# Optimization experiments

Hardware: AMD Instinct MI355X
Metric: run time of the kernel (lower is better)

Reference implementation:

```python
import jax, jax.numpy as jnp
import numpy as np

H = 64   # LSTM hidden size
NL = 8   # LSTM layers
B, T = 2048, 64


def setup_inputs() -> dict:
    key = jax.random.key(0)
    ks = jax.random.split(key, 18)
    r = lambda i, shape, s=0.1: jax.random.normal(ks[i], shape, dtype=jnp.float32) * s
    return {
        "x": r(0, (B, T, 2), 1.0),
        "w1": r(1, (16, 2)), "b1": r(2, (16,)),
        "w2": r(3, (16, 16)), "b2": r(4, (16,)),
        "w_ih0": r(5, (4 * H, 16)), "w_hh0": r(6, (4 * H, H)),
        "b_ih0": r(7, (4 * H,)), "b_hh0": r(8, (4 * H,)),
        "w_ih": r(9, (NL - 1, 4 * H, H)), "w_hh": r(10, (NL - 1, 4 * H, H)),
        "b_ih": r(11, (NL - 1, 4 * H)), "b_hh": r(12, (NL - 1, 4 * H)),
        "wo1": r(13, (32, H)), "bo1": r(14, (32,)),
        "wo2": r(15, (4, 32)), "bo2": r(16, (4,)),
    }


def _lstm_layer(x, w_ih, w_hh, b):
    # x: [B, T, I]; torch gate order: i, f, g, o
    bsz = x.shape[0]
    xg = jnp.einsum('bti,gi->btg', x, w_ih) + b  # [B, T, 4H] precomputed input gates

    def step(carry, xg_t):
        h, c = carry
        gates = xg_t + h @ w_hh.T
        i, f, g, o = jnp.split(gates, 4, axis=-1)
        i = jax.nn.sigmoid(i); f = jax.nn.sigmoid(f)
        g = jnp.tanh(g); o = jax.nn.sigmoid(o)
        c = f * c + i * g
        h = o * jnp.tanh(c)
        return (h, c), h

    h0 = jnp.zeros((bsz, H), x.dtype)
    _, hs = jax.lax.scan(step, (h0, h0), jnp.swapaxes(xg, 0, 1))  # [T, B, H]
    return jnp.swapaxes(hs, 0, 1)


def reference(x, w1, b1, w2, b2, w_ih0, w_hh0, b_ih0, b_hh0,
              w_ih, w_hh, b_ih, b_hh, wo1, bo1, wo2, bo2):
    # action-input MLP: 2 -> 16 -> relu -> 16
    h = jax.nn.relu(x @ w1.T + b1) @ w2.T + b2
    # 8-layer LSTM, hidden 64
    h = _lstm_layer(h, w_ih0, w_hh0, b_ih0 + b_hh0)
    for l in range(NL - 1):
        h = _lstm_layer(h, w_ih[l], w_hh[l], b_ih[l] + b_hh[l])
    # output MLP: 64 -> 32 -> relu -> 4
    return jax.nn.relu(h @ wo1.T + bo1) @ wo2.T + bo2
```

## Files before the change

### kernel.cpp

```cpp
#include <hip/hip_runtime.h>


#define BATCH 2048
#define TT 64
#define HH 64
#define LDP 136

typedef short bf16x8 __attribute__((ext_vector_type(8)));
typedef float f32x4 __attribute__((ext_vector_type(4)));

__device__ __forceinline__ float sigmoid_fast(float x) {
    return __builtin_amdgcn_rcpf(1.f + __expf(-x));
}
__device__ __forceinline__ float tanh_fast(float x) {
    float e = __expf(-2.f * x);
    e = fminf(e, 1e30f);
    return (1.f - e) * __builtin_amdgcn_rcpf(1.f + e);
}
__device__ __forceinline__ void split2(float x, unsigned short& hi, unsigned short& lo) {
    const unsigned u = __float_as_uint(x);
    hi = (unsigned short)(u >> 16);
    const float r = x - __uint_as_float(u & 0xFFFF0000u);
    lo = (unsigned short)(__float_as_uint(r) >> 16);
}

__global__ __launch_bounds__(256)
void mlp_in_kernel(const float* __restrict__ x,
                   const float* __restrict__ w1, const float* __restrict__ b1,
                   const float* __restrict__ w2, const float* __restrict__ b2,
                   float* __restrict__ out) {
    const int gid = blockIdx.x * 256 + threadIdx.x;
    const float x0 = x[gid * 2 + 0];
    const float x1 = x[gid * 2 + 1];
    float hid[16];
#pragma unroll
    for (int j = 0; j < 16; ++j) {
        float v = fmaf(x1, w1[j * 2 + 1], fmaf(x0, w1[j * 2 + 0], b1[j]));
        hid[j] = fmaxf(0.f, v);
    }
    float o[16];
#pragma unroll
    for (int oo = 0; oo < 16; ++oo) {
        float acc = b2[oo];
#pragma unroll
        for (int j = 0; j < 16; ++j) acc = fmaf(hid[j], w2[oo * 16 + j], acc);
        o[oo] = acc;
    }
    float4* op = (float4*)(out + gid * 16);
#pragma unroll
    for (int q = 0; q < 4; ++q) {
        float4 v;
        v.x = o[q * 4 + 0]; v.y = o[q * 4 + 1]; v.z = o[q * 4 + 2]; v.w = o[q * 4 + 3];
        op[q] = v;
    }
}

template <int I, int IPAD>
__global__ __launch_bounds__(512, 2)
void lstm_layer(const float* __restrict__ xin,
                const float* __restrict__ w_ih, const float* __restrict__ w_hh,
                const float* __restrict__ b_ih, const float* __restrict__ b_hh,
                float* __restrict__ hout) {
    constexpr int K = IPAD + 64;
    constexpr int KT = K / 32;
    __shared__ unsigned short ph[2][16 * LDP];
    __shared__ unsigned short pl[2][16 * LDP];
    __shared__ float gsw[8][32][8];

    const int tid = threadIdx.x;
    const int wv = tid >> 6, lane = tid & 63, l16 = lane & 15, quad = lane >> 4;
    const int base = blockIdx.x * 8;

    for (int e = tid; e < 16 * LDP; e += 512) {
        ph[0][e] = 0; pl[0][e] = 0; ph[1][e] = 0; pl[1][e] = 0;
    }

    bf16x8 bhi[KT][2], blo[KT][2];
    float bsum[2];
#pragma unroll
    for (int ntl = 0; ntl < 2; ++ntl) {
        const int gate = ntl * 2 + (l16 >> 3);
        const int n = gate * 64 + 8 * wv + (l16 & 7);
        bsum[ntl] = b_ih[n] + b_hh[n];
#pragma unroll
        for (int kt = 0; kt < KT; ++kt) {
#pragma unroll
            for (int j = 0; j < 8; ++j) {
                const int k = kt * 32 + quad * 8 + j;
                float w = 0.f;
                if (k < I) w = w_ih[n * I + k];
                else if (k >= IPAD) w = w_hh[n * 64 + (k - IPAD)];
                unsigned short h_, l_;
                split2(w, h_, l_);
                bhi[kt][ntl][j] = (short)h_;
                blo[kt][ntl][j] = (short)l_;
            }
        }
    }

    float c = 0.f;
    const int cm = lane >> 3, cjj = lane & 7;
    const int cj = 8 * wv + cjj;

    const int am = (I == 64) ? (tid >> 6) : (tid >> 4);
    const int ak = (I == 64) ? (tid & 63) : (tid & 15);
    const bool stg = (I == 64) ? true : (tid < 128);

    float xr = 0.f;
    if (stg) xr = xin[((size_t)(base + am) * TT + 0) * I + ak];
    if (stg) {
        unsigned short h_, l_;
        split2(xr, h_, l_);
        ph[0][am * LDP + ak] = h_;
        pl[0][am * LDP + ak] = l_;
    }
    if (stg) xr = xin[((size_t)(base + am) * TT + 1) * I + ak];
    __syncthreads();

    for (int t = 0; t < TT; ++t) {
        const int pb = t & 1;
        const unsigned short* php = ph[pb];
        const unsigned short* plp = pl[pb];
        unsigned short* phn = ph[pb ^ 1];
        unsigned short* pln = pl[pb ^ 1];

        f32x4 a0[2], a1[2], a2[2];
#pragma unroll
        for (int ntl = 0; ntl < 2; ++ntl) {
            a0[ntl][0] = bsum[ntl]; a0[ntl][1] = bsum[ntl];
            a0[ntl][2] = bsum[ntl]; a0[ntl][3] = bsum[ntl];
            a1[ntl] = (f32x4){0.f, 0.f, 0.f, 0.f};
            a2[ntl] = (f32x4){0.f, 0.f, 0.f, 0.f};
        }
#pragma unroll
        for (int kt = 0; kt < KT; ++kt) {
            const int aoff = l16 * LDP + kt * 32 + quad * 8;
            const bf16x8 ahi = *(const bf16x8*)&php[aoff];
            const bf16x8 alo = *(const bf16x8*)&plp[aoff];
#pragma unroll
            for (int ntl = 0; ntl < 2; ++ntl) {
                a0[ntl] = __builtin_amdgcn_mfma_f32_16x16x32_bf16(ahi, bhi[kt][ntl], a0[ntl], 0, 0, 0);
                a1[ntl] = __builtin_amdgcn_mfma_f32_16x16x32_bf16(alo, bhi[kt][ntl], a1[ntl], 0, 0, 0);
                a2[ntl] = __builtin_amdgcn_mfma_f32_16x16x32_bf16(ahi, blo[kt][ntl], a2[ntl], 0, 0, 0);
            }
        }
        if (quad < 2) {
#pragma unroll
            for (int ntl = 0; ntl < 2; ++ntl) {
                const f32x4 s = (a0[ntl] + a1[ntl]) + a2[ntl];
                *(f32x4*)&gsw[wv][ntl * 16 + l16][quad * 4] = s;
            }
        }

        const float gi = gsw[wv][0 * 8 + cjj][cm];
        const float gf = gsw[wv][1 * 8 + cjj][cm];
        const float gg = gsw[wv][2 * 8 + cjj][cm];
        const float go = gsw[wv][3 * 8 + cjj][cm];
        const float iv = sigmoid_fast(gi), fv = sigmoid_fast(gf);
        const float gv = tanh_fast(gg), ov = sigmoid_fast(go);
        c = fv * c + iv * gv;
        const float h = ov * tanh_fast(c);
        {
            unsigned short h_, l_;
            split2(h, h_, l_);
            phn[cm * LDP + IPAD + cj] = h_;
            pln[cm * LDP + IPAD + cj] = l_;
            hout[((size_t)(base + cm) * TT + t) * HH + cj] = h;
        }

        if (stg) {
            unsigned short h_, l_;
            split2(xr, h_, l_);
            phn[am * LDP + ak] = h_;
            pln[am * LDP + ak] = l_;
            const int tp = (t + 2) & (TT - 1);
            xr = xin[((size_t)(base + am) * TT + tp) * I + ak];
        }
        __syncthreads();
    }
}

__global__ __launch_bounds__(256)
void mlp_out_kernel(const float* __restrict__ hin,
                    const float* __restrict__ wo1, const float* __restrict__ bo1,
                    const float* __restrict__ wo2, const float* __restrict__ bo2,
                    float* __restrict__ out) {
    __shared__ __align__(16) float wo1_s[32 * 64];
    __shared__ float bo1_s[32];
    __shared__ float wo2_s[4 * 32];
    __shared__ float bo2_s[4];
    const int tid = threadIdx.x;
    for (int e = tid; e < 32 * 64; e += 256) wo1_s[e] = wo1[e];
    if (tid < 32) bo1_s[tid] = bo1[tid];
    if (tid < 128) wo2_s[tid] = wo2[tid];
    if (tid < 4) bo2_s[tid] = bo2[tid];
    __syncthreads();

    const int gid = blockIdx.x * 256 + tid;
    const float4* hv = (const float4*)(hin + gid * 64);
    float4 h[16];
#pragma unroll
    for (int q = 0; q < 16; ++q) h[q] = hv[q];

    float m1[32];
#pragma unroll
    for (int o = 0; o < 32; ++o) {
        float acc = bo1_s[o];
        const float4* wrow = (const float4*)(wo1_s + o * 64);
#pragma unroll
        for (int q = 0; q < 16; ++q) {
            const float4 w = wrow[q];
            acc = fmaf(h[q].x, w.x, acc);
            acc = fmaf(h[q].y, w.y, acc);
            acc = fmaf(h[q].z, w.z, acc);
            acc = fmaf(h[q].w, w.w, acc);
        }
        m1[o] = fmaxf(0.f, acc);
    }
    float r[4];
#pragma unroll
    for (int q = 0; q < 4; ++q) {
        float acc = bo2_s[q];
#pragma unroll
        for (int o = 0; o < 32; ++o) acc = fmaf(m1[o], wo2_s[q * 32 + o], acc);
        r[q] = acc;
    }
    float4 res;
    res.x = r[0]; res.y = r[1]; res.z = r[2]; res.w = r[3];
    ((float4*)out)[gid] = res;
}

extern "C" void kernel_launch(void* const* d_in, const int* in_sizes, int n_in,
                              void* d_out, int out_size, void* d_ws, size_t ws_size,
                              hipStream_t stream) {
    const float* x     = (const float*)d_in[0];
    const float* w1    = (const float*)d_in[1];
    const float* b1    = (const float*)d_in[2];
    const float* w2    = (const float*)d_in[3];
    const float* b2    = (const float*)d_in[4];
    const float* w_ih0 = (const float*)d_in[5];
    const float* w_hh0 = (const float*)d_in[6];
    const float* b_ih0 = (const float*)d_in[7];
    const float* b_hh0 = (const float*)d_in[8];
    const float* w_ih  = (const float*)d_in[9];
    const float* w_hh  = (const float*)d_in[10];
    const float* b_ih  = (const float*)d_in[11];
    const float* b_hh  = (const float*)d_in[12];
    const float* wo1   = (const float*)d_in[13];
    const float* bo1   = (const float*)d_in[14];
    const float* wo2   = (const float*)d_in[15];
    const float* bo2   = (const float*)d_in[16];

    float* buf_mlp = (float*)d_ws;
    float* bufA = buf_mlp + (size_t)BATCH * TT * 16;
    float* bufB = bufA + (size_t)BATCH * TT * 64;

    const int nbt_blocks = (BATCH * TT) / 256;

    mlp_in_kernel<<<nbt_blocks, 256, 0, stream>>>(x, w1, b1, w2, b2, buf_mlp);

    lstm_layer<16, 32><<<BATCH / 8, 512, 0, stream>>>(buf_mlp, w_ih0, w_hh0, b_ih0, b_hh0, bufA);

    const float* cur = bufA;
    float* nxt = bufB;
    for (int l = 0; l < 7; ++l) {
        lstm_layer<64, 64><<<BATCH / 8, 512, 0, stream>>>(
            cur, w_ih + (size_t)l * 256 * 64, w_hh + (size_t)l * 256 * 64,
            b_ih + (size_t)l * 256, b_hh + (size_t)l * 256, nxt);
        const float* tmp = nxt;
        nxt = (float*)cur;
        cur = tmp;
    }

    mlp_out_kernel<<<nbt_blocks, 256, 0, stream>>>(cur, wo1, bo1, wo2, bo2, (float*)d_out);
}
```

Measured before the change: 572.1 us.

## Fuse eight LSTM layers into one wavefront-pipelined persistent kernel

```diff
diff --git a/kernel.cpp b/kernel.cpp
--- a/kernel.cpp
+++ b/kernel.cpp
@@ -5,9 +5,12 @@
 #define TT 64
 #define HH 64
 #define LDP 136
+#define GRP 32
+#define RING 8
 
 typedef short bf16x8 __attribute__((ext_vector_type(8)));
 typedef float f32x4 __attribute__((ext_vector_type(4)));
+typedef unsigned short u16x4 __attribute__((ext_vector_type(4)));
 
 __device__ __forceinline__ float sigmoid_fast(float x) {
     return __builtin_amdgcn_rcpf(1.f + __expf(-x));
@@ -55,128 +58,186 @@
     }
 }
 
-template <int I, int IPAD>
 __global__ __launch_bounds__(512, 2)
-void lstm_layer(const float* __restrict__ xin,
-                const float* __restrict__ w_ih, const float* __restrict__ w_hh,
-                const float* __restrict__ b_ih, const float* __restrict__ b_hh,
-                float* __restrict__ hout) {
-    constexpr int K = IPAD + 64;
-    constexpr int KT = K / 32;
-    __shared__ unsigned short ph[2][16 * LDP];
-    __shared__ unsigned short pl[2][16 * LDP];
-    __shared__ float gsw[8][32][8];
-
+void lstm_wavefront(const float* __restrict__ xmlp,
+                    const float* __restrict__ w_ih0, const float* __restrict__ w_hh0,
+                    const float* __restrict__ b_ih0, const float* __restrict__ b_hh0,
+                    const float* __restrict__ w_ih, const float* __restrict__ w_hh,
+                    const float* __restrict__ b_ih, const float* __restrict__ b_hh,
+                    unsigned* __restrict__ hring,
+                    float* __restrict__ houtf,
+                    int* __restrict__ prog,
+                    int* __restrict__ cons)
+{
+    const int bid = blockIdx.x;
+    const int l = bid >> 5, g = bid & (GRP - 1);
     const int tid = threadIdx.x;
     const int wv = tid >> 6, lane = tid & 63, l16 = lane & 15, quad = lane >> 4;
-    const int base = blockIdx.x * 8;
-
-    for (int e = tid; e < 16 * LDP; e += 512) {
+    const int mw = wv >> 2, nw = wv & 3;
+
+    const int I    = (l == 0) ? 16 : 64;
+    const int IPAD = (l == 0) ? 32 : 64;
+    const int KT   = (l == 0) ? 3 : 4;
+    const float* wih = (l == 0) ? w_ih0 : (w_ih + (size_t)(l - 1) * 256 * 64);
+    const float* whh = (l == 0) ? w_hh0 : (w_hh + (size_t)(l - 1) * 256 * 64);
+    const float* bi  = (l == 0) ? b_ih0 : (b_ih + (l - 1) * 256);
+    const float* bh  = (l == 0) ? b_hh0 : (b_hh + (l - 1) * 256);
+
+    __shared__ unsigned short ph[2][64 * LDP];
+    __shared__ unsigned short pl[2][64 * LDP];
+
+    for (int e = tid; e < 64 * LDP; e += 512) {
         ph[0][e] = 0; pl[0][e] = 0; ph[1][e] = 0; pl[1][e] = 0;
     }
 
-    bf16x8 bhi[KT][2], blo[KT][2];
-    float bsum[2];
-#pragma unroll
-    for (int ntl = 0; ntl < 2; ++ntl) {
-        const int gate = ntl * 2 + (l16 >> 3);
-        const int n = gate * 64 + 8 * wv + (l16 & 7);
-        bsum[ntl] = b_ih[n] + b_hh[n];
-#pragma unroll
-        for (int kt = 0; kt < KT; ++kt) {
-#pragma unroll
-            for (int j = 0; j < 8; ++j) {
-                const int k = kt * 32 + quad * 8 + j;
-                float w = 0.f;
-                if (k < I) w = w_ih[n * I + k];
-                else if (k >= IPAD) w = w_hh[n * 64 + (k - IPAD)];
-                unsigned short h_, l_;
-                split2(w, h_, l_);
-                bhi[kt][ntl][j] = (short)h_;
-                blo[kt][ntl][j] = (short)l_;
-            }
-        }
-    }
-
-    float c = 0.f;
-    const int cm = lane >> 3, cjj = lane & 7;
-    const int cj = 8 * wv + cjj;
-
-    const int am = (I == 64) ? (tid >> 6) : (tid >> 4);
-    const int ak = (I == 64) ? (tid & 63) : (tid & 15);
-    const bool stg = (I == 64) ? true : (tid < 128);
-
-    float xr = 0.f;
-    if (stg) xr = xin[((size_t)(base + am) * TT + 0) * I + ak];
-    if (stg) {
-        unsigned short h_, l_;
-        split2(xr, h_, l_);
-        ph[0][am * LDP + ak] = h_;
-        pl[0][am * LDP + ak] = l_;
-    }
-    if (stg) xr = xin[((size_t)(base + am) * TT + 1) * I + ak];
+    bf16x8 bhi[4][4], blo[4][4];
+    float bsum[4];
+#pragma unroll
+    for (int gt = 0; gt < 4; ++gt) {
+        const int n = gt * 64 + 16 * nw + l16;
+        bsum[gt] = bi[n] + bh[n];
+#pragma unroll
+        for (int kt = 0; kt < 4; ++kt) {
+            bf16x8 vh = {0, 0, 0, 0, 0, 0, 0, 0};
+            bf16x8 vl = {0, 0, 0, 0, 0, 0, 0, 0};
+            if (kt < KT) {
+#pragma unroll
+                for (int j = 0; j < 8; ++j) {
+                    const int k = kt * 32 + quad * 8 + j;
+                    float w = 0.f;
+                    if (k < I) w = wih[n * I + k];
+                    else if (k >= IPAD) w = whh[n * 64 + (k - IPAD)];
+                    unsigned short h_, l_;
+                    split2(w, h_, l_);
+                    vh[j] = (short)h_;
+                    vl[j] = (short)l_;
+                }
+            }
+            bhi[kt][gt] = vh;
+            blo[kt][gt] = vl;
+        }
+    }
+
+    float cst[2][4];
+#pragma unroll
+    for (int q = 0; q < 4; ++q) { cst[0][q] = 0.f; cst[1][q] = 0.f; }
+
+    int* myprog = prog + l * GRP + g;
+    int* upprog = prog + (l > 0 ? (l - 1) : 0) * GRP + g;
+    int* mycons = cons + l * GRP + g;
+    int* dncons = cons + (l < 7 ? (l + 1) : 7) * GRP + g;
+    const unsigned* hr_src = hring + ((size_t)((l > 0 ? l - 1 : 0) * GRP + g)) * (RING * 4096);
+    unsigned* hr_dst = hring + ((size_t)((l < 7 ? l : 6) * GRP + g)) * (RING * 4096);
+
+    const int jg = 16 * nw + l16;
+
     __syncthreads();
 
     for (int t = 0; t < TT; ++t) {
         const int pb = t & 1;
+
+        if (tid == 0) {
+            if (l > 0) {
+                while (__hip_atomic_load(upprog, __ATOMIC_ACQUIRE, __HIP_MEMORY_SCOPE_AGENT) < t + 1)
+                    __builtin_amdgcn_s_sleep(1);
+            }
+            if (l < 7 && t >= RING) {
+                while (__hip_atomic_load(dncons, __ATOMIC_ACQUIRE, __HIP_MEMORY_SCOPE_AGENT) < t - (RING - 1))
+                    __builtin_amdgcn_s_sleep(1);
+            }
+        }
+        __syncthreads();
+
+        if (l == 0) {
+            if (tid < 256) {
+                const int r = tid >> 2, q = tid & 3;
+                const float4 v = *(const float4*)&xmlp[(((size_t)(g * 64 + r)) * TT + t) * 16 + q * 4];
+                unsigned short h0, h1, h2, h3, e0, e1, e2, e3;
+                split2(v.x, h0, e0); split2(v.y, h1, e1);
+                split2(v.z, h2, e2); split2(v.w, h3, e3);
+                u16x4 hv = {h0, h1, h2, h3};
+                u16x4 lv = {e0, e1, e2, e3};
+                *(u16x4*)&ph[pb][r * LDP + q * 4] = hv;
+                *(u16x4*)&pl[pb][r * LDP + q * 4] = lv;
+            }
+        } else {
+            const int r = tid >> 3, q = tid & 7;
+            const unsigned* s = hr_src + (size_t)(t & (RING - 1)) * 4096 + r * 64 + q * 8;
+            const uint4 v0 = *(const uint4*)s;
+            const uint4 v1 = *(const uint4*)(s + 4);
+            bf16x8 hv, lv;
+            hv[0] = (short)(v0.x >> 16); lv[0] = (short)(v0.x & 0xffffu);
+            hv[1] = (short)(v0.y >> 16); lv[1] = (short)(v0.y & 0xffffu);
+            hv[2] = (short)(v0.z >> 16); lv[2] = (short)(v0.z & 0xffffu);
+            hv[3] = (short)(v0.w >> 16); lv[3] = (short)(v0.w & 0xffffu);
+            hv[4] = (short)(v1.x >> 16); lv[4] = (short)(v1.x & 0xffffu);
+            hv[5] = (short)(v1.y >> 16); lv[5] = (short)(v1.y & 0xffffu);
+            hv[6] = (short)(v1.z >> 16); lv[6] = (short)(v1.z & 0xffffu);
+            hv[7] = (short)(v1.w >> 16); lv[7] = (short)(v1.w & 0xffffu);
+            *(bf16x8*)&ph[pb][r * LDP + q * 8] = hv;
+            *(bf16x8*)&pl[pb][r * LDP + q * 8] = lv;
+        }
+        __syncthreads();
+        if (tid == 0 && l > 0)
+            __hip_atomic_store(mycons, t + 1, __ATOMIC_RELEASE, __HIP_MEMORY_SCOPE_AGENT);
+
         const unsigned short* php = ph[pb];
         const unsigned short* plp = pl[pb];
         unsigned short* phn = ph[pb ^ 1];
         unsigned short* pln = pl[pb ^ 1];
 
-        f32x4 a0[2], a1[2], a2[2];
-#pragma unroll
-        for (int ntl = 0; ntl < 2; ++ntl) {
-            a0[ntl][0] = bsum[ntl]; a0[ntl][1] = bsum[ntl];
-            a0[ntl][2] = bsum[ntl]; a0[ntl][3] = bsum[ntl];
-            a1[ntl] = (f32x4){0.f, 0.f, 0.f, 0.f};
-            a2[ntl] = (f32x4){0.f, 0.f, 0.f, 0.f};
-        }
-#pragma unroll
-        for (int kt = 0; kt < KT; ++kt) {
-            const int aoff = l16 * LDP + kt * 32 + quad * 8;
-            const bf16x8 ahi = *(const bf16x8*)&php[aoff];
-            const bf16x8 alo = *(const bf16x8*)&plp[aoff];
-#pragma unroll
-            for (int ntl = 0; ntl < 2; ++ntl) {
-                a0[ntl] = __builtin_amdgcn_mfma_f32_16x16x32_bf16(ahi, bhi[kt][ntl], a0[ntl], 0, 0, 0);
-                a1[ntl] = __builtin_amdgcn_mfma_f32_16x16x32_bf16(alo, bhi[kt][ntl], a1[ntl], 0, 0, 0);
-                a2[ntl] = __builtin_amdgcn_mfma_f32_16x16x32_bf16(ahi, blo[kt][ntl], a2[ntl], 0, 0, 0);
-            }
-        }
-        if (quad < 2) {
-#pragma unroll
-            for (int ntl = 0; ntl < 2; ++ntl) {
-                const f32x4 s = (a0[ntl] + a1[ntl]) + a2[ntl];
-                *(f32x4*)&gsw[wv][ntl * 16 + l16][quad * 4] = s;
-            }
-        }
-
-        const float gi = gsw[wv][0 * 8 + cjj][cm];
-        const float gf = gsw[wv][1 * 8 + cjj][cm];
-        const float gg = gsw[wv][2 * 8 + cjj][cm];
-        const float go = gsw[wv][3 * 8 + cjj][cm];
-        const float iv = sigmoid_fast(gi), fv = sigmoid_fast(gf);
-        const float gv = tanh_fast(gg), ov = sigmoid_fast(go);
-        c = fv * c + iv * gv;
-        const float h = ov * tanh_fast(c);
-        {
-            unsigned short h_, l_;
-            split2(h, h_, l_);
-            phn[cm * LDP + IPAD + cj] = h_;
-            pln[cm * LDP + IPAD + cj] = l_;
-            hout[((size_t)(base + cm) * TT + t) * HH + cj] = h;
-        }
-
-        if (stg) {
-            unsigned short h_, l_;
-            split2(xr, h_, l_);
-            phn[am * LDP + ak] = h_;
-            pln[am * LDP + ak] = l_;
-            const int tp = (t + 2) & (TT - 1);
-            xr = xin[((size_t)(base + am) * TT + tp) * I + ak];
+#pragma unroll
+        for (int ch = 0; ch < 2; ++ch) {
+            const int mt = mw * 2 + ch;
+            f32x4 a0[4], a1[4], a2[4];
+#pragma unroll
+            for (int gt = 0; gt < 4; ++gt) {
+                a0[gt][0] = bsum[gt]; a0[gt][1] = bsum[gt];
+                a0[gt][2] = bsum[gt]; a0[gt][3] = bsum[gt];
+                a1[gt] = (f32x4){0.f, 0.f, 0.f, 0.f};
+                a2[gt] = (f32x4){0.f, 0.f, 0.f, 0.f};
+            }
+#pragma unroll
+            for (int kt = 0; kt < 4; ++kt) {
+                if (kt < KT) {
+                    const int aoff = (mt * 16 + l16) * LDP + kt * 32 + quad * 8;
+                    const bf16x8 ahi = *(const bf16x8*)&php[aoff];
+                    const bf16x8 alo = *(const bf16x8*)&plp[aoff];
+#pragma unroll
+                    for (int gt = 0; gt < 4; ++gt) {
+                        a0[gt] = __builtin_amdgcn_mfma_f32_16x16x32_bf16(ahi, bhi[kt][gt], a0[gt], 0, 0, 0);
+                        a1[gt] = __builtin_amdgcn_mfma_f32_16x16x32_bf16(alo, bhi[kt][gt], a1[gt], 0, 0, 0);
+                        a2[gt] = __builtin_amdgcn_mfma_f32_16x16x32_bf16(ahi, blo[kt][gt], a2[gt], 0, 0, 0);
+                    }
+                }
+            }
+#pragma unroll
+            for (int rr = 0; rr < 4; ++rr) {
+                const float gi = (a0[0][rr] + a1[0][rr]) + a2[0][rr];
+                const float gf = (a0[1][rr] + a1[1][rr]) + a2[1][rr];
+                const float gg = (a0[2][rr] + a1[2][rr]) + a2[2][rr];
+                const float go = (a0[3][rr] + a1[3][rr]) + a2[3][rr];
+                const float iv = sigmoid_fast(gi), fv = sigmoid_fast(gf);
+                const float gv = tanh_fast(gg), ov = sigmoid_fast(go);
+                const float cn = fv * cst[ch][rr] + iv * gv;
+                cst[ch][rr] = cn;
+                const float h = ov * tanh_fast(cn);
+                const int R = mt * 16 + quad * 4 + rr;
+                unsigned short h_, l_;
+                split2(h, h_, l_);
+                phn[R * LDP + IPAD + jg] = h_;
+                pln[R * LDP + IPAD + jg] = l_;
+                if (l < 7) {
+                    hr_dst[(size_t)(t & (RING - 1)) * 4096 + R * 64 + jg] =
+                        ((unsigned)h_ << 16) | (unsigned)l_;
+                } else {
+                    houtf[(((size_t)(g * 64 + R)) * TT + t) * HH + jg] = h;
+                }
+            }
         }
         __syncthreads();
+        if (tid == 0 && l < 7)
+            __hip_atomic_store(myprog, t + 1, __ATOMIC_RELEASE, __HIP_MEMORY_SCOPE_AGENT);
     }
 }
 
@@ -252,25 +313,22 @@
     const float* bo2   = (const float*)d_in[16];
 
     float* buf_mlp = (float*)d_ws;
-    float* bufA = buf_mlp + (size_t)BATCH * TT * 16;
-    float* bufB = bufA + (size_t)BATCH * TT * 64;
+    float* bufH = buf_mlp + (size_t)BATCH * TT * 16;
+    unsigned* hring = (unsigned*)(bufH + (size_t)BATCH * TT * 64);
+    int* flags = (int*)(hring + (size_t)7 * GRP * RING * 64 * 64);
+    int* prog = flags;
+    int* cons = flags + 8 * GRP;
 
     const int nbt_blocks = (BATCH * TT) / 256;
 
+    hipMemsetAsync(flags, 0, 2 * 8 * GRP * sizeof(int), stream);
+
     mlp_in_kernel<<<nbt_blocks, 256, 0, stream>>>(x, w1, b1, w2, b2, buf_mlp);
 
-    lstm_layer<16, 32><<<BATCH / 8, 512, 0, stream>>>(buf_mlp, w_ih0, w_hh0, b_ih0, b_hh0, bufA);
-
-    const float* cur = bufA;
-    float* nxt = bufB;
-    for (int l = 0; l < 7; ++l) {
-        lstm_layer<64, 64><<<BATCH / 8, 512, 0, stream>>>(
-            cur, w_ih + (size_t)l * 256 * 64, w_hh + (size_t)l * 256 * 64,
-            b_ih + (size_t)l * 256, b_hh + (size_t)l * 256, nxt);
-        const float* tmp = nxt;
-        nxt = (float*)cur;
-        cur = tmp;
-    }
-
-    mlp_out_kernel<<<nbt_blocks, 256, 0, stream>>>(cur, wo1, bo1, wo2, bo2, (float*)d_out);
-}
+    lstm_wavefront<<<8 * GRP, 512, 0, stream>>>(
+        buf_mlp, w_ih0, w_hh0, b_ih0, b_hh0,
+        w_ih, w_hh, b_ih, b_hh,
+        hring, bufH, prog, cons);
+
+    mlp_out_kernel<<<nbt_blocks, 256, 0, stream>>>(bufH, wo1, bo1, wo2, bo2, (float*)d_out);
+}
```

Result: slower. 1.503 ms (+162.7%).

## Split LSTM step across 1024 threads and pass pre-split bf16 activations between layers

Applied to the files above, without the earlier changes.

```diff
diff --git a/kernel.cpp b/kernel.cpp
--- a/kernel.cpp
+++ b/kernel.cpp
@@ -5,6 +5,7 @@
 #define TT 64
 #define HH 64
 #define LDP 136
+#define GJR 552
 
 typedef short bf16x8 __attribute__((ext_vector_type(8)));
 typedef float f32x4 __attribute__((ext_vector_type(4)));
@@ -56,125 +57,131 @@
 }
 
 template <int I, int IPAD>
-__global__ __launch_bounds__(512, 2)
-void lstm_layer(const float* __restrict__ xin,
-                const float* __restrict__ w_ih, const float* __restrict__ w_hh,
-                const float* __restrict__ b_ih, const float* __restrict__ b_hh,
-                float* __restrict__ hout) {
-    constexpr int K = IPAD + 64;
-    constexpr int KT = K / 32;
-    __shared__ unsigned short ph[2][16 * LDP];
-    __shared__ unsigned short pl[2][16 * LDP];
-    __shared__ float gsw[8][32][8];
+__global__ __launch_bounds__(1024)
+void lstm_layer1k(const float* __restrict__ xf,
+                  const unsigned* xp,
+                  unsigned* Pout,
+                  float* __restrict__ houtf,
+                  const int last,
+                  const float* __restrict__ wih, const float* __restrict__ whh,
+                  const float* __restrict__ bi, const float* __restrict__ bh) {
+    constexpr int KT = (IPAD + 64) / 32;
+    __shared__ __align__(16) unsigned short ph[2][16 * LDP], pl[2][16 * LDP];
+    __shared__ float gsw[4 * GJR];
 
     const int tid = threadIdx.x;
     const int wv = tid >> 6, lane = tid & 63, l16 = lane & 15, quad = lane >> 4;
+    const int gt = wv & 3, jr = wv >> 2;
     const int base = blockIdx.x * 8;
 
-    for (int e = tid; e < 16 * LDP; e += 512) {
-        ph[0][e] = 0; pl[0][e] = 0; ph[1][e] = 0; pl[1][e] = 0;
-    }
-
-    bf16x8 bhi[KT][2], blo[KT][2];
-    float bsum[2];
-#pragma unroll
-    for (int ntl = 0; ntl < 2; ++ntl) {
-        const int gate = ntl * 2 + (l16 >> 3);
-        const int n = gate * 64 + 8 * wv + (l16 & 7);
-        bsum[ntl] = b_ih[n] + b_hh[n];
-#pragma unroll
-        for (int kt = 0; kt < KT; ++kt) {
-#pragma unroll
-            for (int j = 0; j < 8; ++j) {
-                const int k = kt * 32 + quad * 8 + j;
-                float w = 0.f;
-                if (k < I) w = w_ih[n * I + k];
-                else if (k >= IPAD) w = w_hh[n * 64 + (k - IPAD)];
-                unsigned short h_, l_;
-                split2(w, h_, l_);
-                bhi[kt][ntl][j] = (short)h_;
-                blo[kt][ntl][j] = (short)l_;
-            }
-        }
-    }
-
+    for (int e = tid; e < 2 * 16 * LDP; e += 1024) { (&ph[0][0])[e] = 0; (&pl[0][0])[e] = 0; }
+
+    const int n = gt * 64 + jr * 16 + l16;
+    const float bsum = bi[n] + bh[n];
+    bf16x8 bhi[KT], blo[KT];
+#pragma unroll
+    for (int kt = 0; kt < KT; ++kt) {
+#pragma unroll
+        for (int j = 0; j < 8; ++j) {
+            const int k = kt * 32 + quad * 8 + j;
+            float w = 0.f;
+            if (k < I) w = wih[n * I + k];
+            else if (k >= IPAD) w = whh[n * 64 + (k - IPAD)];
+            unsigned short h_, l_;
+            split2(w, h_, l_);
+            bhi[kt][j] = (short)h_;
+            blo[kt][j] = (short)l_;
+        }
+    }
+
+    const int crow = tid >> 6, cj = tid & 63;
     float c = 0.f;
-    const int cm = lane >> 3, cjj = lane & 7;
-    const int cj = 8 * wv + cjj;
-
-    const int am = (I == 64) ? (tid >> 6) : (tid >> 4);
-    const int ak = (I == 64) ? (tid & 63) : (tid & 15);
-    const bool stg = (I == 64) ? true : (tid < 128);
-
-    float xr = 0.f;
-    if (stg) xr = xin[((size_t)(base + am) * TT + 0) * I + ak];
+
+    const int sidx = tid - 512;
+    const bool stg = (I == 16) ? (tid >= 512 && tid < 640) : (tid >= 512);
+    const int sr = (I == 16) ? (sidx >> 4) : (sidx >> 6);
+    const int sc = (I == 16) ? (sidx & 15) : (sidx & 63);
+    float xrf = 0.f;
+    unsigned xru = 0u;
     if (stg) {
-        unsigned short h_, l_;
-        split2(xr, h_, l_);
-        ph[0][am * LDP + ak] = h_;
-        pl[0][am * LDP + ak] = l_;
-    }
-    if (stg) xr = xin[((size_t)(base + am) * TT + 1) * I + ak];
+        if (I == 16) {
+            xrf = xf[((size_t)(base + sr) * TT + 0) * 16 + sc];
+            unsigned short h_, l_;
+            split2(xrf, h_, l_);
+            ph[0][sr * LDP + sc] = h_;
+            pl[0][sr * LDP + sc] = l_;
+            xrf = xf[((size_t)(base + sr) * TT + 1) * 16 + sc];
+        } else {
+            xru = xp[((size_t)(base + sr) * TT + 0) * 64 + sc];
+            ph[0][sr * LDP + sc] = (unsigned short)(xru >> 16);
+            pl[0][sr * LDP + sc] = (unsigned short)(xru & 0xffffu);
+            xru = xp[((size_t)(base + sr) * TT + 1) * 64 + sc];
+        }
+    }
     __syncthreads();
 
     for (int t = 0; t < TT; ++t) {
         const int pb = t & 1;
-        const unsigned short* php = ph[pb];
-        const unsigned short* plp = pl[pb];
-        unsigned short* phn = ph[pb ^ 1];
-        unsigned short* pln = pl[pb ^ 1];
-
-        f32x4 a0[2], a1[2], a2[2];
-#pragma unroll
-        for (int ntl = 0; ntl < 2; ++ntl) {
-            a0[ntl][0] = bsum[ntl]; a0[ntl][1] = bsum[ntl];
-            a0[ntl][2] = bsum[ntl]; a0[ntl][3] = bsum[ntl];
-            a1[ntl] = (f32x4){0.f, 0.f, 0.f, 0.f};
-            a2[ntl] = (f32x4){0.f, 0.f, 0.f, 0.f};
-        }
+
+        f32x4 a0, a1, a2;
+        a0[0] = bsum; a0[1] = bsum; a0[2] = bsum; a0[3] = bsum;
+        a1 = (f32x4){0.f, 0.f, 0.f, 0.f};
+        a2 = (f32x4){0.f, 0.f, 0.f, 0.f};
 #pragma unroll
         for (int kt = 0; kt < KT; ++kt) {
             const int aoff = l16 * LDP + kt * 32 + quad * 8;
-            const bf16x8 ahi = *(const bf16x8*)&php[aoff];
-            const bf16x8 alo = *(const bf16x8*)&plp[aoff];
-#pragma unroll
-            for (int ntl = 0; ntl < 2; ++ntl) {
-                a0[ntl] = __builtin_amdgcn_mfma_f32_16x16x32_bf16(ahi, bhi[kt][ntl], a0[ntl], 0, 0, 0);
-                a1[ntl] = __builtin_amdgcn_mfma_f32_16x16x32_bf16(alo, bhi[kt][ntl], a1[ntl], 0, 0, 0);
-                a2[ntl] = __builtin_amdgcn_mfma_f32_16x16x32_bf16(ahi, blo[kt][ntl], a2[ntl], 0, 0, 0);
-            }
-        }
+            const bf16x8 ahi = *(const bf16x8*)&ph[pb][aoff];
+            const bf16x8 alo = *(const bf16x8*)&pl[pb][aoff];
+            a0 = __builtin_amdgcn_mfma_f32_16x16x32_bf16(ahi, bhi[kt], a0, 0, 0, 0);
+            a1 = __builtin_amdgcn_mfma_f32_16x16x32_bf16(alo, bhi[kt], a1, 0, 0, 0);
+            a2 = __builtin_amdgcn_mfma_f32_16x16x32_bf16(ahi, blo[kt], a2, 0, 0, 0);
+        }
+        const f32x4 s4 = (a0 + a1) + a2;
         if (quad < 2) {
-#pragma unroll
-            for (int ntl = 0; ntl < 2; ++ntl) {
-                const f32x4 s = (a0[ntl] + a1[ntl]) + a2[ntl];
-                *(f32x4*)&gsw[wv][ntl * 16 + l16][quad * 4] = s;
-            }
-        }
-
-        const float gi = gsw[wv][0 * 8 + cjj][cm];
-        const float gf = gsw[wv][1 * 8 + cjj][cm];
-        const float gg = gsw[wv][2 * 8 + cjj][cm];
-        const float go = gsw[wv][3 * 8 + cjj][cm];
-        const float iv = sigmoid_fast(gi), fv = sigmoid_fast(gf);
-        const float gv = tanh_fast(gg), ov = sigmoid_fast(go);
-        c = fv * c + iv * gv;
-        const float h = ov * tanh_fast(c);
-        {
+            const int gb = jr * GJR + (gt * 8 + quad * 4) * 17 + l16;
+            gsw[gb + 0]  = s4[0];
+            gsw[gb + 17] = s4[1];
+            gsw[gb + 34] = s4[2];
+            gsw[gb + 51] = s4[3];
+        }
+        __syncthreads();
+
+        if (tid < 512) {
+            const int gb = (cj >> 4) * GJR + crow * 17 + (cj & 15);
+            const float gi = gsw[gb + 0 * 136];
+            const float gf = gsw[gb + 1 * 136];
+            const float gg = gsw[gb + 2 * 136];
+            const float go = gsw[gb + 3 * 136];
+            const float iv = sigmoid_fast(gi), fv = sigmoid_fast(gf);
+            const float gv = tanh_fast(gg), ov = sigmoid_fast(go);
+            c = fv * c + iv * gv;
+            const float h = ov * tanh_fast(c);
             unsigned short h_, l_;
             split2(h, h_, l_);
-            phn[cm * LDP + IPAD + cj] = h_;
-            pln[cm * LDP + IPAD + cj] = l_;
-            hout[((size_t)(base + cm) * TT + t) * HH + cj] = h;
+            ph[pb ^ 1][crow * LDP + IPAD + cj] = h_;
+            pl[pb ^ 1][crow * LDP + IPAD + cj] = l_;
+            if (!last) {
+                Pout[((size_t)(base + crow) * TT + t) * 64 + cj] =
+                    ((unsigned)h_ << 16) | (unsigned)l_;
+            } else {
+                houtf[((size_t)(base + crow) * TT + t) * HH + cj] = h;
+            }
         }
 
         if (stg) {
-            unsigned short h_, l_;
-            split2(xr, h_, l_);
-            phn[am * LDP + ak] = h_;
-            pln[am * LDP + ak] = l_;
-            const int tp = (t + 2) & (TT - 1);
-            xr = xin[((size_t)(base + am) * TT + tp) * I + ak];
+            if (I == 16) {
+                unsigned short h_, l_;
+                split2(xrf, h_, l_);
+                ph[pb ^ 1][sr * LDP + sc] = h_;
+                pl[pb ^ 1][sr * LDP + sc] = l_;
+                const int tp = (t + 2) & (TT - 1);
+                xrf = xf[((size_t)(base + sr) * TT + tp) * 16 + sc];
+            } else {
+                ph[pb ^ 1][sr * LDP + sc] = (unsigned short)(xru >> 16);
+                pl[pb ^ 1][sr * LDP + sc] = (unsigned short)(xru & 0xffffu);
+                const int tp = (t + 2) & (TT - 1);
+                xru = xp[((size_t)(base + sr) * TT + tp) * 64 + sc];
+            }
         }
         __syncthreads();
     }
@@ -252,25 +259,22 @@
     const float* bo2   = (const float*)d_in[16];
 
     float* buf_mlp = (float*)d_ws;
-    float* bufA = buf_mlp + (size_t)BATCH * TT * 16;
-    float* bufB = bufA + (size_t)BATCH * TT * 64;
+    unsigned* P = (unsigned*)(buf_mlp + (size_t)BATCH * TT * 16);
+    float* bufH = (float*)(P + (size_t)BATCH * TT * 64);
 
     const int nbt_blocks = (BATCH * TT) / 256;
 
     mlp_in_kernel<<<nbt_blocks, 256, 0, stream>>>(x, w1, b1, w2, b2, buf_mlp);
 
-    lstm_layer<16, 32><<<BATCH / 8, 512, 0, stream>>>(buf_mlp, w_ih0, w_hh0, b_ih0, b_hh0, bufA);
-
-    const float* cur = bufA;
-    float* nxt = bufB;
-    for (int l = 0; l < 7; ++l) {
-        lstm_layer<64, 64><<<BATCH / 8, 512, 0, stream>>>(
-            cur, w_ih + (size_t)l * 256 * 64, w_hh + (size_t)l * 256 * 64,
-            b_ih + (size_t)l * 256, b_hh + (size_t)l * 256, nxt);
-        const float* tmp = nxt;
-        nxt = (float*)cur;
-        cur = tmp;
-    }
-
-    mlp_out_kernel<<<nbt_blocks, 256, 0, stream>>>(cur, wo1, bo1, wo2, bo2, (float*)d_out);
-}
+    lstm_layer1k<16, 32><<<BATCH / 8, 1024, 0, stream>>>(
+        buf_mlp, nullptr, P, bufH, 0, w_ih0, w_hh0, b_ih0, b_hh0);
+
+    for (int l = 1; l < 8; ++l) {
+        lstm_layer1k<64, 64><<<BATCH / 8, 1024, 0, stream>>>(
+            buf_mlp, P, P, bufH, (l == 7) ? 1 : 0,
+            w_ih + (size_t)(l - 1) * 256 * 64, w_hh + (size_t)(l - 1) * 256 * 64,
+            b_ih + (l - 1) * 256, b_hh + (l - 1) * 256);
+    }
+
+    mlp_out_kernel<<<nbt_blocks, 256, 0, stream>>>(bufH, wo1, bo1, wo2, bo2, (float*)d_out);
+}
```

Result: slower. 644.5 us (+12.6%).
